# Optimization experiments

Hardware: AMD Instinct MI355X
Metric: run time of the kernel (lower is better)

The kernel has to match this reference:

```python
import jax, jax.numpy as jnp
import numpy as np

B, T, D, H = 2, 2048, 1024, 16
HS = D // H  # head_size = 64
DFF = 4 * D


def setup_inputs() -> dict:
    key = jax.random.key(0)
    ks = jax.random.split(key, 12)
    s = 0.02
    return {
        "x": jax.random.normal(ks[0], (B, T, D), dtype=jnp.float32),
        "Wq": jax.random.normal(ks[1], (D, D), dtype=jnp.float32) * s,
        "Wk": jax.random.normal(ks[2], (D, D), dtype=jnp.float32) * s,
        "Wv": jax.random.normal(ks[3], (D, D), dtype=jnp.float32) * s,
        "Wo": jax.random.normal(ks[4], (D, D), dtype=jnp.float32) * s,
        "bo": jnp.zeros((D,), dtype=jnp.float32),
        "W1": jax.random.normal(ks[5], (D, DFF), dtype=jnp.float32) * s,
        "b1": jnp.zeros((DFF,), dtype=jnp.float32),
        "W2": jax.random.normal(ks[6], (DFF, D), dtype=jnp.float32) * s,
        "b2": jnp.zeros((D,), dtype=jnp.float32),
        "g1": jnp.ones((D,), dtype=jnp.float32),
        "be1": jnp.zeros((D,), dtype=jnp.float32),
        "g2": jnp.ones((D,), dtype=jnp.float32),
        "be2": jnp.zeros((D,), dtype=jnp.float32),
    }


def layer_norm(x, g, b, eps=1e-5):
    mu = jnp.mean(x, axis=-1, keepdims=True)
    var = jnp.var(x, axis=-1, keepdims=True)
    return (x - mu) * jax.lax.rsqrt(var + eps) * g + b


def attention(x, Wq, Wk, Wv, Wo, bo):
    # x: [B,T,D] -> q,k,v: [B,H,T,HS]
    def split_heads(y):
        return y.reshape(B, T, H, HS).transpose(0, 2, 1, 3)
    q = split_heads(x @ Wq)
    k = split_heads(x @ Wk)
    v = split_heads(x @ Wv)
    scores = jnp.einsum("bhqd,bhkd->bhqk", q, k) / jnp.sqrt(jnp.float32(HS))
    causal = jnp.tril(jnp.ones((T, T), dtype=bool))
    scores = jnp.where(causal, scores, -jnp.inf)
    probs = jax.nn.softmax(scores, axis=-1)
    out = jnp.einsum("bhqk,bhkd->bhqd", probs, v)
    out = out.transpose(0, 2, 1, 3).reshape(B, T, D)
    return out @ Wo + bo


def reference(x, Wq, Wk, Wv, Wo, bo, W1, b1, W2, b2, g1, be1, g2, be2):
    x = x + attention(layer_norm(x, g1, be1), Wq, Wk, Wv, Wo, bo)
    h = layer_norm(x, g2, be2)
    x = x + (jax.nn.relu(h @ W1 + b1) @ W2 + b2)
    return x
```

## Files before the change

### kernel.cpp

```cpp
#include <hip/hip_runtime.h>
#include <stdint.h>

#define Bc   2
#define Tc   2048
#define Dc   1024
#define Hc   16
#define HSc  64
#define DFFc 4096
#define Mc   (Bc * Tc)

using f32x4 = __attribute__((ext_vector_type(4))) float;
using s16x8 = __attribute__((ext_vector_type(8))) short;

__device__ __forceinline__ ushort f2bf(float f) {
  union { float f; uint32_t u; } v; v.f = f;
  uint32_t r = (v.u + 0x7FFFu + ((v.u >> 16) & 1u)) >> 16;
  return (ushort)r;
}
__device__ __forceinline__ float bf2f(ushort u) {
  union { uint32_t u; float f; } v; v.u = ((uint32_t)u) << 16;
  return v.f;
}
__device__ __forceinline__ float wredsum(float v) {
#pragma unroll
  for (int o = 32; o > 0; o >>= 1) v += __shfl_down(v, o);
  return v;
}

__device__ __forceinline__ void gload16(const ushort* g, ushort* l) {
  __builtin_amdgcn_global_load_lds(
      (const __attribute__((address_space(1))) void*)g,
      (__attribute__((address_space(3))) void*)l, 16, 0, 0);
}

__global__ __launch_bounds__(256) void tcast_kernel(const float* __restrict__ src,
                                                    ushort* __restrict__ dst,
                                                    int K, int N) {
  __shared__ float t[32][33];
  const int tid = threadIdx.x;
  const int n0 = blockIdx.x * 32, k0 = blockIdx.y * 32;
  const int r = tid >> 3, c4 = (tid & 7) * 4;
  const float4 v = *(const float4*)&src[(size_t)(k0 + r) * N + n0 + c4];
  t[r][c4] = v.x; t[r][c4 + 1] = v.y; t[r][c4 + 2] = v.z; t[r][c4 + 3] = v.w;
  __syncthreads();
  ushort4 o;
  o.x = f2bf(t[c4 + 0][r]); o.y = f2bf(t[c4 + 1][r]);
  o.z = f2bf(t[c4 + 2][r]); o.w = f2bf(t[c4 + 3][r]);
  *(ushort4*)&dst[(size_t)(n0 + r) * K + k0 + c4] = o;
}

__global__ __launch_bounds__(256) void ln_kernel(const float* __restrict__ x,
                                                 const float* __restrict__ g,
                                                 const float* __restrict__ b,
                                                 ushort* __restrict__ out) {
  const int row = blockIdx.x;
  const int tid = threadIdx.x;
  const int lane = tid & 63, wave = tid >> 6;
  const float4 v = ((const float4*)(x + (size_t)row * Dc))[tid];
  float s  = v.x + v.y + v.z + v.w;
  float s2 = v.x * v.x + v.y * v.y + v.z * v.z + v.w * v.w;
  __shared__ float rs[4], rs2[4];
  s = wredsum(s); s2 = wredsum(s2);
  if (lane == 0) { rs[wave] = s; rs2[wave] = s2; }
  __syncthreads();
  const float S  = rs[0] + rs[1] + rs[2] + rs[3];
  const float S2 = rs2[0] + rs2[1] + rs2[2] + rs2[3];
  const float mu = S * (1.f / (float)Dc);
  const float rstd = rsqrtf(S2 * (1.f / (float)Dc) - mu * mu + 1e-5f);
  const float4 gv = ((const float4*)g)[tid];
  const float4 bv = ((const float4*)b)[tid];
  ushort4 o;
  o.x = f2bf((v.x - mu) * rstd * gv.x + bv.x);
  o.y = f2bf((v.y - mu) * rstd * gv.y + bv.y);
  o.z = f2bf((v.z - mu) * rstd * gv.z + bv.z);
  o.w = f2bf((v.w - mu) * rstd * gv.w + bv.w);
  ((ushort4*)(out + (size_t)row * Dc))[tid] = o;
}

template <int BM, int NSPLIT, int OUT_BF16, int RELU, int BIAS, int RES, int QKVSPLIT>
__global__ __launch_bounds__(256) void gemm3_kernel(
    const ushort* __restrict__ A, const ushort* __restrict__ Bt,
    const float* __restrict__ bias, const float* __restrict__ res,
    void* __restrict__ C0, void* __restrict__ C1, void* __restrict__ C2,
    int M, int N, int K) {
  constexpr int MF = BM / 32;
  __shared__ __align__(16) ushort As[BM * 64];
  __shared__ __align__(16) ushort Bs[128 * 64];
  const int tid = threadIdx.x;
  const int lane = tid & 63, w = tid >> 6;
  const int wm = w >> 1, wn = w & 1;
  const int row0 = blockIdx.x * BM, col0 = blockIdx.y * 128;
  const int fr = lane & 15, fg = lane >> 4;
  const int kbeg = (NSPLIT > 1) ? blockIdx.z * (K / NSPLIT) : 0;
  const int kend = (NSPLIT > 1) ? kbeg + K / NSPLIT : K;

  f32x4 acc[MF][4] = {};

  for (int k0 = kbeg; k0 < kend; k0 += 64) {
#pragma unroll
    for (int i = 0; i < BM * 8 / 256; i++) {
      const int c = i * 256 + tid;
      const int r = c >> 3, j = c & 7;
      gload16(A + (size_t)(row0 + r) * K + k0 + ((j ^ (r & 7)) << 3),
              As + (i * 256 + w * 64) * 8);
    }
#pragma unroll
    for (int i = 0; i < 4; i++) {
      const int c = i * 256 + tid;
      const int r = c >> 3, j = c & 7;
      gload16(Bt + (size_t)(col0 + r) * K + k0 + ((j ^ (r & 7)) << 3),
              Bs + (i * 256 + w * 64) * 8);
    }
    __syncthreads();

#pragma unroll
    for (int kk = 0; kk < 2; kk++) {
      const int js = ((kk * 4 + fg) ^ (fr & 7)) << 3;
      s16x8 af[MF], bfr[4];
#pragma unroll
      for (int m = 0; m < MF; m++)
        af[m] = *(const s16x8*)&As[(wm * (BM / 2) + m * 16 + fr) * 64 + js];
#pragma unroll
      for (int n = 0; n < 4; n++)
        bfr[n] = *(const s16x8*)&Bs[(wn * 64 + n * 16 + fr) * 64 + js];
#pragma unroll
      for (int m = 0; m < MF; m++)
#pragma unroll
        for (int n = 0; n < 4; n++)
          acc[m][n] = __builtin_amdgcn_mfma_f32_16x16x32_bf16(af[m], bfr[n], acc[m][n], 0, 0, 0);
    }
    __syncthreads();
  }

  if (NSPLIT > 1) {
    float* P = (float*)C0 + (size_t)blockIdx.z * M * N;
#pragma unroll
    for (int m = 0; m < MF; m++)
#pragma unroll
      for (int n = 0; n < 4; n++)
#pragma unroll
        for (int i = 0; i < 4; i++) {
          const int r = row0 + wm * (BM / 2) + m * 16 + fg * 4 + i;
          const int c = col0 + n * 16 + wn * 64 + fr;
          P[(size_t)r * N + c] = acc[m][n][i];
        }
    return;
  }

  void* Cb = C0;
  int cbase = col0;
  if (QKVSPLIT) {
    const int which = col0 >> 10;
    Cb = (which == 0) ? C0 : (which == 1) ? C1 : C2;
    cbase = col0 & 1023;
  }
  const int NW = QKVSPLIT ? 1024 : N;
#pragma unroll
  for (int m = 0; m < MF; m++) {
#pragma unroll
    for (int n = 0; n < 4; n++) {
#pragma unroll
      for (int i = 0; i < 4; i++) {
        const int r = row0 + wm * (BM / 2) + m * 16 + fg * 4 + i;
        const int c = cbase + wn * 64 + n * 16 + fr;
        float v = acc[m][n][i];
        if (BIAS) v += bias[col0 - cbase + c];
        if (RELU) v = fmaxf(v, 0.f);
        if (RES)  v += res[(size_t)r * NW + c];
        if (OUT_BF16) ((ushort*)Cb)[(size_t)r * NW + c] = f2bf(v);
        else          ((float*)Cb)[(size_t)r * NW + c] = v;
      }
    }
  }
}

__global__ __launch_bounds__(256) void sum2_kernel(const float* __restrict__ p0,
                                                   const float* __restrict__ p1,
                                                   const float* __restrict__ bias,
                                                   const float* __restrict__ res,
                                                   float* __restrict__ out) {
  const size_t i = ((size_t)blockIdx.x * 256 + threadIdx.x) * 4;
  const float4 a = *(const float4*)(p0 + i);
  const float4 b = *(const float4*)(p1 + i);
  const float4 r = *(const float4*)(res + i);
  const float4 bs = *(const float4*)(bias + (i & 1023));
  float4 o;
  o.x = a.x + b.x + bs.x + r.x;
  o.y = a.y + b.y + bs.y + r.y;
  o.z = a.z + b.z + bs.z + r.z;
  o.w = a.w + b.w + bs.w + r.w;
  *(float4*)(out + i) = o;
}

__global__ __launch_bounds__(512) void fattn2_kernel(const ushort* __restrict__ Q,
                                                     const ushort* __restrict__ K,
                                                     const ushort* __restrict__ V,
                                                     ushort* __restrict__ O) {
  __shared__ __align__(16) ushort Kl[64][72];
  __shared__ __align__(16) ushort Vt[64][72];
  __shared__ __align__(16) ushort Pl[8][8][16][8];

  const int tid = threadIdx.x;
  const int lane = tid & 63, w = tid >> 6;
  const int fr = lane & 15, fg = lane >> 4;

  const int bh  = blockIdx.x & 31;
  const int qbi = blockIdx.x >> 5;
  const int qb  = (qbi & 1) ? ((qbi - 1) >> 1) : (15 - (qbi >> 1));
  const int h = bh & 15, b = bh >> 4;
  const int q0 = qb * 128;
  const size_t hbase = (size_t)b * Tc * Dc + (size_t)h * HSc;

  s16x8 qf0, qf1;
  {
    const ushort* qp = Q + hbase + (size_t)(q0 + w * 16 + fr) * Dc + fg * 8;
    qf0 = *(const s16x8*)(qp);
    qf1 = *(const s16x8*)(qp + 32);
  }

  const int kkey = tid >> 3, kd8 = (tid & 7) * 8;
  const int vkey = tid & 63, vd8 = (tid >> 6) * 8;

  const int nt = 2 * qb + 2;
  uint4 kreg = *(const uint4*)(K + hbase + (size_t)kkey * Dc + kd8);
  uint4 vreg = *(const uint4*)(V + hbase + (size_t)vkey * Dc + vd8);

  f32x4 acc[4] = {};
  float ps[4] = {0.f, 0.f, 0.f, 0.f};
  const float C = 0.18033688f;

  for (int kt = 0; kt < nt; kt++) {
    *(uint4*)&Kl[kkey][kd8] = kreg;
    {
      union { uint4 v; ushort u[8]; } t; t.v = vreg;
#pragma unroll
      for (int j = 0; j < 8; j++) Vt[vd8 + j][vkey] = t.u[j];
    }
    __syncthreads();

    if (kt + 1 < nt) {
      kreg = *(const uint4*)(K + hbase + (size_t)((kt + 1) * 64 + kkey) * Dc + kd8);
      vreg = *(const uint4*)(V + hbase + (size_t)((kt + 1) * 64 + vkey) * Dc + vd8);
    }

    const bool skip = (kt * 64 > q0 + w * 16 + 15);
    if (!skip) {
      f32x4 s[4] = {};
#pragma unroll
      for (int kf = 0; kf < 4; kf++) {
        const s16x8 k0 = *(const s16x8*)&Kl[kf * 16 + fr][fg * 8];
        const s16x8 k1 = *(const s16x8*)&Kl[kf * 16 + fr][32 + fg * 8];
        s[kf] = __builtin_amdgcn_mfma_f32_16x16x32_bf16(qf0, k0, s[kf], 0, 0, 0);
        s[kf] = __builtin_amdgcn_mfma_f32_16x16x32_bf16(qf1, k1, s[kf], 0, 0, 0);
      }
      const bool diag = (kt * 64 + 63 > q0 + w * 16);
#pragma unroll
      for (int kf = 0; kf < 4; kf++) {
#pragma unroll
        for (int i = 0; i < 4; i++) {
          float p = exp2f(s[kf][i] * C);
          if (diag) {
            const int kg = kt * 64 + kf * 16 + fr;
            const int qg = q0 + w * 16 + fg * 4 + i;
            if (kg > qg) p = 0.f;
          }
          ps[i] += p;
          Pl[w][2 * kf + (fr >> 3)][fg * 4 + i][fr & 7] = f2bf(p);
        }
      }
      const s16x8 pa0 = *(const s16x8*)&Pl[w][fg][fr][0];
      const s16x8 pa1 = *(const s16x8*)&Pl[w][4 + fg][fr][0];
#pragma unroll
      for (int df = 0; df < 4; df++) {
        const s16x8 v0 = *(const s16x8*)&Vt[df * 16 + fr][fg * 8];
        const s16x8 v1 = *(const s16x8*)&Vt[df * 16 + fr][32 + fg * 8];
        acc[df] = __builtin_amdgcn_mfma_f32_16x16x32_bf16(pa0, v0, acc[df], 0, 0, 0);
        acc[df] = __builtin_amdgcn_mfma_f32_16x16x32_bf16(pa1, v1, acc[df], 0, 0, 0);
      }
    }
    __syncthreads();
  }

#pragma unroll
  for (int i = 0; i < 4; i++) {
    float v = ps[i];
#pragma unroll
    for (int o = 1; o < 16; o <<= 1) v += __shfl_xor(v, o);
    const float inv = 1.f / v;
    ushort* op = O + hbase + (size_t)(q0 + w * 16 + fg * 4 + i) * Dc;
#pragma unroll
    for (int df = 0; df < 4; df++) op[df * 16 + fr] = f2bf(acc[df][i] * inv);
  }
}

extern "C" void kernel_launch(void* const* d_in, const int* in_sizes, int n_in,
                              void* d_out, int out_size, void* d_ws, size_t ws_size,
                              hipStream_t stream) {
  const float* x   = (const float*)d_in[0];
  const float* Wq  = (const float*)d_in[1];
  const float* Wk  = (const float*)d_in[2];
  const float* Wv  = (const float*)d_in[3];
  const float* Wo  = (const float*)d_in[4];
  const float* bo  = (const float*)d_in[5];
  const float* W1  = (const float*)d_in[6];
  const float* b1  = (const float*)d_in[7];
  const float* W2  = (const float*)d_in[8];
  const float* b2  = (const float*)d_in[9];
  const float* g1  = (const float*)d_in[10];
  const float* be1 = (const float*)d_in[11];
  const float* g2  = (const float*)d_in[12];
  const float* be2 = (const float*)d_in[13];

  char* ws = (char*)d_ws;
  const size_t MB = 1ull << 20;
  ushort* ln1   = (ushort*)(ws + 0 * MB);
  ushort* qb    = (ushort*)(ws + 8 * MB);
  ushort* kb    = (ushort*)(ws + 16 * MB);
  ushort* vb    = (ushort*)(ws + 24 * MB);
  ushort* wqkvt = (ushort*)(ws + 32 * MB);
  ushort* wot   = (ushort*)(ws + 38 * MB);
  ushort* w1t   = (ushort*)(ws + 40 * MB);
  ushort* w2t   = (ushort*)(ws + 48 * MB);
  float*  x1    = (float*)(ws + 56 * MB);
  ushort* hb    = (ushort*)(ws + 72 * MB);
  float*  fpart = (float*)(ws + 0 * MB);

  tcast_kernel<<<dim3(32, 32), 256, 0, stream>>>(Wq, wqkvt, Dc, Dc);
  tcast_kernel<<<dim3(32, 32), 256, 0, stream>>>(Wk, wqkvt + 1024 * 1024, Dc, Dc);
  tcast_kernel<<<dim3(32, 32), 256, 0, stream>>>(Wv, wqkvt + 2048 * 1024, Dc, Dc);
  tcast_kernel<<<dim3(32, 32), 256, 0, stream>>>(Wo, wot, Dc, Dc);
  tcast_kernel<<<dim3(128, 32), 256, 0, stream>>>(W1, w1t, Dc, DFFc);
  tcast_kernel<<<dim3(32, 128), 256, 0, stream>>>(W2, w2t, DFFc, Dc);

  ln_kernel<<<Mc, 256, 0, stream>>>(x, g1, be1, ln1);

  gemm3_kernel<128, 1, 1, 0, 0, 0, 1><<<dim3(32, 24), 256, 0, stream>>>(
      ln1, wqkvt, nullptr, nullptr, qb, kb, vb, Mc, 3072, Dc);

  fattn2_kernel<<<512, 512, 0, stream>>>(qb, kb, vb, ln1);

  gemm3_kernel<64, 1, 0, 0, 1, 1, 0><<<dim3(64, 8), 256, 0, stream>>>(
      ln1, wot, bo, x, x1, nullptr, nullptr, Mc, Dc, Dc);

  ln_kernel<<<Mc, 256, 0, stream>>>(x1, g2, be2, qb);

  gemm3_kernel<128, 1, 1, 1, 1, 0, 0><<<dim3(32, 32), 256, 0, stream>>>(
      qb, w1t, b1, nullptr, hb, nullptr, nullptr, Mc, DFFc, Dc);

  gemm3_kernel<128, 2, 0, 0, 0, 0, 0><<<dim3(32, 8, 2), 256, 0, stream>>>(
      hb, w2t, nullptr, nullptr, fpart, nullptr, nullptr, Mc, Dc, DFFc);
  sum2_kernel<<<4096, 256, 0, stream>>>(fpart, fpart + (size_t)Mc * Dc, b2, x1,
                                        (float*)d_out);
}
```

Before: 249.2 us.

## Split attention over key range into two partial passes plus merge kernel

The attention kernel now splits each query block's causal key range into two halves handled by separate workgroups, which doubles the grid. Partial unnormalized outputs and row sums go to fp32 workspace, and a new merge kernel combines them and normalizes to bf16. It also double-buffers the K/V LDS tiles to remove one barrier per iteration, swaps the QK MFMA operand order so each lane holds a query row, packs P with v_cvt_pk_bf16_f32, and raises wave priority around the MFMA sections. The cost is extra fp32 partial traffic, one extra launch, and uneven split sizes for small query blocks.

```diff
diff --git a/kernel.cpp b/kernel.cpp
--- a/kernel.cpp
+++ b/kernel.cpp
@@ -20,6 +20,11 @@
 __device__ __forceinline__ float bf2f(ushort u) {
   union { uint32_t u; float f; } v; v.u = ((uint32_t)u) << 16;
   return v.f;
+}
+__device__ __forceinline__ uint32_t cvtpk(float a, float b) {
+  uint32_t r;
+  asm volatile("v_cvt_pk_bf16_f32 %0, %1, %2" : "=v"(r) : "v"(a), "v"(b));
+  return r;
 }
 __device__ __forceinline__ float wredsum(float v) {
 #pragma unroll
@@ -192,21 +197,23 @@
   *(float4*)(out + i) = o;
 }
 
-__global__ __launch_bounds__(512) void fattn2_kernel(const ushort* __restrict__ Q,
+__global__ __launch_bounds__(512) void fattn3_kernel(const ushort* __restrict__ Q,
                                                      const ushort* __restrict__ K,
                                                      const ushort* __restrict__ V,
-                                                     ushort* __restrict__ O) {
-  __shared__ __align__(16) ushort Kl[64][72];
-  __shared__ __align__(16) ushort Vt[64][72];
-  __shared__ __align__(16) ushort Pl[8][8][16][8];
+                                                     float* __restrict__ pacc,
+                                                     float* __restrict__ pl) {
+  __shared__ __align__(16) ushort Kl[2][64][72];
+  __shared__ __align__(16) ushort Vt[2][64][72];
+  __shared__ __align__(16) uint32_t Pu[8][512];
 
   const int tid = threadIdx.x;
   const int lane = tid & 63, w = tid >> 6;
   const int fr = lane & 15, fg = lane >> 4;
 
-  const int bh  = blockIdx.x & 31;
-  const int qbi = blockIdx.x >> 5;
-  const int qb  = (qbi & 1) ? ((qbi - 1) >> 1) : (15 - (qbi >> 1));
+  const int bh   = blockIdx.x & 31;
+  const int rest = blockIdx.x >> 5;
+  const int qb   = 15 - (rest >> 1);
+  const int z    = rest & 1;
   const int h = bh & 15, b = bh >> 4;
   const int q0 = qb * 128;
   const size_t hbase = (size_t)b * Tc * Dc + (size_t)h * HSc;
@@ -221,76 +228,108 @@
   const int kkey = tid >> 3, kd8 = (tid & 7) * 8;
   const int vkey = tid & 63, vd8 = (tid >> 6) * 8;
 
-  const int nt = 2 * qb + 2;
-  uint4 kreg = *(const uint4*)(K + hbase + (size_t)kkey * Dc + kd8);
-  uint4 vreg = *(const uint4*)(V + hbase + (size_t)vkey * Dc + vd8);
+  const int t0 = z * (qb + 1), t1 = (z + 1) * (qb + 1);
+  uint4 kreg = *(const uint4*)(K + hbase + (size_t)(t0 * 64 + kkey) * Dc + kd8);
+  uint4 vreg = *(const uint4*)(V + hbase + (size_t)(t0 * 64 + vkey) * Dc + vd8);
 
   f32x4 acc[4] = {};
-  float ps[4] = {0.f, 0.f, 0.f, 0.f};
-  const float C = 0.18033688f;
-
-  for (int kt = 0; kt < nt; kt++) {
-    *(uint4*)&Kl[kkey][kd8] = kreg;
+  float ps = 0.f;
+  const float Cs = 0.18033688f;
+
+  for (int kt = t0; kt < t1; kt++) {
+    const int cur = (kt - t0) & 1;
+    *(uint4*)&Kl[cur][kkey][kd8] = kreg;
     {
       union { uint4 v; ushort u[8]; } t; t.v = vreg;
 #pragma unroll
-      for (int j = 0; j < 8; j++) Vt[vd8 + j][vkey] = t.u[j];
-    }
-    __syncthreads();
-
-    if (kt + 1 < nt) {
+      for (int j = 0; j < 8; j++) Vt[cur][vd8 + j][vkey] = t.u[j];
+    }
+    if (kt + 1 < t1) {
       kreg = *(const uint4*)(K + hbase + (size_t)((kt + 1) * 64 + kkey) * Dc + kd8);
       vreg = *(const uint4*)(V + hbase + (size_t)((kt + 1) * 64 + vkey) * Dc + vd8);
     }
+    __syncthreads();
 
     const bool skip = (kt * 64 > q0 + w * 16 + 15);
     if (!skip) {
       f32x4 s[4] = {};
+      __builtin_amdgcn_s_setprio(1);
 #pragma unroll
       for (int kf = 0; kf < 4; kf++) {
-        const s16x8 k0 = *(const s16x8*)&Kl[kf * 16 + fr][fg * 8];
-        const s16x8 k1 = *(const s16x8*)&Kl[kf * 16 + fr][32 + fg * 8];
-        s[kf] = __builtin_amdgcn_mfma_f32_16x16x32_bf16(qf0, k0, s[kf], 0, 0, 0);
-        s[kf] = __builtin_amdgcn_mfma_f32_16x16x32_bf16(qf1, k1, s[kf], 0, 0, 0);
+        const s16x8 k0 = *(const s16x8*)&Kl[cur][kf * 16 + fr][fg * 8];
+        const s16x8 k1 = *(const s16x8*)&Kl[cur][kf * 16 + fr][32 + fg * 8];
+        s[kf] = __builtin_amdgcn_mfma_f32_16x16x32_bf16(k0, qf0, s[kf], 0, 0, 0);
+        s[kf] = __builtin_amdgcn_mfma_f32_16x16x32_bf16(k1, qf1, s[kf], 0, 0, 0);
       }
+      __builtin_amdgcn_s_setprio(0);
+
       const bool diag = (kt * 64 + 63 > q0 + w * 16);
+      const int qg = q0 + w * 16 + fr;
 #pragma unroll
       for (int kf = 0; kf < 4; kf++) {
+        float p[4];
 #pragma unroll
         for (int i = 0; i < 4; i++) {
-          float p = exp2f(s[kf][i] * C);
+          p[i] = exp2f(s[kf][i] * Cs);
           if (diag) {
-            const int kg = kt * 64 + kf * 16 + fr;
-            const int qg = q0 + w * 16 + fg * 4 + i;
-            if (kg > qg) p = 0.f;
+            const int kg = kt * 64 + kf * 16 + fg * 4 + i;
+            if (kg > qg) p[i] = 0.f;
           }
-          ps[i] += p;
-          Pl[w][2 * kf + (fr >> 3)][fg * 4 + i][fr & 7] = f2bf(p);
+          ps += p[i];
         }
+        uint2 pk;
+        pk.x = cvtpk(p[0], p[1]);
+        pk.y = cvtpk(p[2], p[3]);
+        *(uint2*)&Pu[w][(2 * kf + (fg >> 1)) * 64 + fr * 4 + (fg & 1) * 2] = pk;
       }
-      const s16x8 pa0 = *(const s16x8*)&Pl[w][fg][fr][0];
-      const s16x8 pa1 = *(const s16x8*)&Pl[w][4 + fg][fr][0];
+
+      const s16x8 pa0 = *(const s16x8*)&Pu[w][fg * 64 + fr * 4];
+      const s16x8 pa1 = *(const s16x8*)&Pu[w][(4 + fg) * 64 + fr * 4];
+      __builtin_amdgcn_s_setprio(1);
 #pragma unroll
       for (int df = 0; df < 4; df++) {
-        const s16x8 v0 = *(const s16x8*)&Vt[df * 16 + fr][fg * 8];
-        const s16x8 v1 = *(const s16x8*)&Vt[df * 16 + fr][32 + fg * 8];
+        const s16x8 v0 = *(const s16x8*)&Vt[cur][df * 16 + fr][fg * 8];
+        const s16x8 v1 = *(const s16x8*)&Vt[cur][df * 16 + fr][32 + fg * 8];
         acc[df] = __builtin_amdgcn_mfma_f32_16x16x32_bf16(pa0, v0, acc[df], 0, 0, 0);
         acc[df] = __builtin_amdgcn_mfma_f32_16x16x32_bf16(pa1, v1, acc[df], 0, 0, 0);
       }
-    }
-    __syncthreads();
-  }
-
+      __builtin_amdgcn_s_setprio(0);
+    }
+  }
+
+  ps += __shfl_xor(ps, 16);
+  ps += __shfl_xor(ps, 32);
+  if (lane < 16)
+    pl[(size_t)z * (32 * 2048) + (size_t)bh * 2048 + q0 + w * 16 + lane] = ps;
+
+  float* pa = pacc + (size_t)z * (32ull * 2048 * 64) + (size_t)bh * 2048 * 64;
 #pragma unroll
   for (int i = 0; i < 4; i++) {
-    float v = ps[i];
-#pragma unroll
-    for (int o = 1; o < 16; o <<= 1) v += __shfl_xor(v, o);
-    const float inv = 1.f / v;
-    ushort* op = O + hbase + (size_t)(q0 + w * 16 + fg * 4 + i) * Dc;
-#pragma unroll
-    for (int df = 0; df < 4; df++) op[df * 16 + fr] = f2bf(acc[df][i] * inv);
-  }
+    const int qr = q0 + w * 16 + fg * 4 + i;
+#pragma unroll
+    for (int df = 0; df < 4; df++)
+      pa[(size_t)qr * 64 + df * 16 + fr] = acc[df][i];
+  }
+}
+
+__global__ __launch_bounds__(256) void amerge_kernel(const float* __restrict__ pacc,
+                                                     const float* __restrict__ pl,
+                                                     ushort* __restrict__ O) {
+  const int g = blockIdx.x * 256 + threadIdx.x;
+  const int d4 = g & 15;
+  const int t  = (g >> 4) & 2047;
+  const int bh = g >> 15;
+  const int h = bh & 15, b = bh >> 4;
+  const size_t base = ((size_t)bh * 2048 + t) * 64 + d4 * 4;
+  const float4 a = *(const float4*)(pacc + base);
+  const float4 c = *(const float4*)(pacc + 32ull * 2048 * 64 + base);
+  const float inv = 1.f / (pl[(size_t)bh * 2048 + t] + pl[32 * 2048 + (size_t)bh * 2048 + t]);
+  ushort4 o;
+  o.x = f2bf((a.x + c.x) * inv);
+  o.y = f2bf((a.y + c.y) * inv);
+  o.z = f2bf((a.z + c.z) * inv);
+  o.w = f2bf((a.w + c.w) * inv);
+  *(ushort4*)&O[((size_t)(b * 2048 + t)) * 1024 + h * 64 + d4 * 4] = o;
 }
 
 extern "C" void kernel_launch(void* const* d_in, const int* in_sizes, int n_in,
@@ -323,6 +362,8 @@
   ushort* w2t   = (ushort*)(ws + 48 * MB);
   float*  x1    = (float*)(ws + 56 * MB);
   ushort* hb    = (ushort*)(ws + 72 * MB);
+  float*  pacc  = (float*)(ws + 56 * MB);
+  float*  plv   = (float*)(ws + 88 * MB);
   float*  fpart = (float*)(ws + 0 * MB);
 
   tcast_kernel<<<dim3(32, 32), 256, 0, stream>>>(Wq, wqkvt, Dc, Dc);
@@ -337,7 +378,8 @@
   gemm3_kernel<128, 1, 1, 0, 0, 0, 1><<<dim3(32, 24), 256, 0, stream>>>(
       ln1, wqkvt, nullptr, nullptr, qb, kb, vb, Mc, 3072, Dc);
 
-  fattn2_kernel<<<512, 512, 0, stream>>>(qb, kb, vb, ln1);
+  fattn3_kernel<<<1024, 512, 0, stream>>>(qb, kb, vb, pacc, plv);
+  amerge_kernel<<<4096, 256, 0, stream>>>(pacc, plv, ln1);
 
   gemm3_kernel<64, 1, 0, 0, 1, 1, 0><<<dim3(64, 8), 256, 0, stream>>>(
       ln1, wot, bo, x, x1, nullptr, nullptr, Mc, Dc, Dc);
```

New measurement: 229.0 us. 8.1% less time.
